# Kernel tuning notes

Measured on AMD Instinct MI355X. Metric: run time of the kernel, lower is better.

## Reference

```python
import jax, jax.numpy as jnp
import numpy as np

N = 200000   # graph nodes
C = 1000     # virtual nodes (clusters)
D = 256      # feature dim (in = hidden = out for this layer)


def setup_inputs() -> dict:
    key = jax.random.key(0)
    ks = jax.random.split(key, 24)
    W = lambda k, shape: jax.random.normal(k, shape, dtype=jnp.float32) * 0.05
    inp = {
        "h": jax.random.normal(ks[0], (N, D), dtype=jnp.float32),
        "g": jax.random.normal(ks[1], (C, D), dtype=jnp.float32),
        "g_hat": jax.random.normal(ks[2], (C, D), dtype=jnp.float32),
        "node2cluster": jax.random.randint(ks[3], (N,), 0, C),
        # AdditiveAttention params (all hidden_dim=D)
        "Wq": W(ks[4], (D, D)),          # query_proj (no bias)
        "Wk": W(ks[5], (D, D)),          # key_proj (no bias)
        "b_attn": jax.random.uniform(ks[6], (D,), jnp.float32, -0.1, 0.1),
        "w_score": W(ks[7], (D,)),       # score_proj weight (D -> 1)
        "b_score": jnp.zeros((), jnp.float32),
        # VNTransmitterUnit.W (D -> D), activation tanh
        "Wv": W(ks[8], (D, D)), "bv": jnp.zeros((D,), jnp.float32),
        # GNTransmitterUnit.F_super (D -> D), tanh
        "Ws": W(ks[9], (D, D)), "bs": jnp.zeros((D,), jnp.float32),
        # gn_merge WarpGateUnit (graph-node side)
        "H1w": W(ks[10], (D, D)), "H1b": jnp.zeros((D,), jnp.float32),
        "G1w": W(ks[11], (D, D)), "G1b": jnp.zeros((D,), jnp.float32),
        # vn_merge WarpGateUnit (virtual-node side)
        "H2w": W(ks[12], (D, D)), "H2b": jnp.zeros((D,), jnp.float32),
        "G2w": W(ks[13], (D, D)), "G2b": jnp.zeros((D,), jnp.float32),
    }
    return inp


def reference(h, g, g_hat, node2cluster,
              Wq, Wk, b_attn, w_score, b_score, Wv, bv, Ws, bs,
              H1w, H1b, G1w, G1b, H2w, H2b, G2w, G2b):
    seg = node2cluster  # (N,) cluster id of each node (the code's vn_index partition)

    # ---- VNTransmitterUnit: segmented additive (Bahdanau) attention, graph -> virtual ----
    # score_proj(tanh(key_proj(cluster_h) + query_proj(g[c]) + bias))
    q = g @ Wq                                             # (C, D)
    k = h @ Wk                                             # (N, D)
    s = jnp.tanh(k + q[seg] + b_attn) @ w_score + b_score  # (N,) per-node score
    # online per-cluster softmax (replaces Python loop over clusters)
    m = jax.ops.segment_max(s, seg, num_segments=C)        # (C,)
    e = jnp.exp(s - m[seg])                                # (N,)
    denom = jax.ops.segment_sum(e, seg, num_segments=C)    # (C,)
    attn = e / denom[seg]                                  # (N,)
    ctx = jax.ops.segment_sum(attn[:, None] * h, seg, num_segments=C)  # (C, D)
    g_trans = jnp.tanh(ctx @ Wv + bv)                      # VNTransmitter: W + tanh

    # ---- GNTransmitterUnit: virtual -> graph, tanh(F_super(g)) then per-node gather ----
    h_trans = jnp.tanh(g @ Ws + bs)                        # (C, D)
    h_trans_n = h_trans[seg]                               # (N, D) index_select by vn_indices[:,1]

    # ---- gn_merge WarpGateUnit: gated fuse on graph nodes ----
    z1 = jax.nn.sigmoid(h @ H1w + H1b + h_trans_n @ G1w + G1b)  # (N, D)
    h_merged = (1.0 - z1) * h + z1 * h_trans_n                   # (N, D)

    # ---- vn_merge WarpGateUnit: gated fuse on virtual nodes (g_hat = vn_update conv out) ----
    z2 = jax.nn.sigmoid(g_trans @ H2w + H2b + g_hat @ G2w + G2b)  # (C, D)
    vx_new = (1.0 - z2) * g_trans + z2 * g_hat                    # (C, D)

    # concat node-side and virtual-side outputs along rows -> (N + C, D)
    return jnp.concatenate([h_merged, vx_new], axis=0)
```

## Files before the change

kernel.cpp:

```cpp
#include <hip/hip_runtime.h>
#include <hip/hip_bf16.h>

#define Nn 200000
#define Cc 1000
#define Dd 256
#define PAD 16
#define NCH7 6250

typedef float f32x16 __attribute__((ext_vector_type(16)));
typedef short bf16x8 __attribute__((ext_vector_type(8)));

#define LOG2E  1.4426950408889634f
#define LOG2E2 2.8853900817779268f

__device__ __forceinline__ unsigned int f2bf(float x){
    union { float f; unsigned int u; } c; c.f = x;
    unsigned int u = c.u;
    u += 0x7fffu + ((u >> 16) & 1u);
    return u >> 16;
}
__device__ __forceinline__ float bf2f(unsigned short b){
    union { unsigned int u; float f; } c; c.u = ((unsigned int)b) << 16;
    return c.f;
}
__device__ __forceinline__ float rcp_(float x){ return __builtin_amdgcn_rcpf(x); }

__global__ void k_prep(const float* __restrict__ Wk, const float* __restrict__ H1w,
                       unsigned short* __restrict__ wfragK, unsigned short* __restrict__ wfragH,
                       int* __restrict__ hist){
    int t = blockIdx.x*256 + threadIdx.x;
    if (t < Cc*PAD) hist[t] = 0;
    int arr = t >> 13;
    int s   = t & 8191;
    int ct  = s >> 10;
    int kk  = (s >> 6) & 15;
    int l   = s & 63;
    int col = ct*32 + (l & 31);
    int k0  = kk*16 + (l >> 5)*8;
    const float* W = arr ? H1w : Wk;
    unsigned short* dst = (arr ? wfragH : wfragK) + (size_t)s*8;
    #pragma unroll
    for (int e = 0; e < 8; ++e) dst[e] = (unsigned short)f2bf(W[(size_t)(k0+e)*Dd + col]);
}

__global__ __launch_bounds__(256)
void k_cluster_prep(const float* __restrict__ g, const float* __restrict__ Wq,
                    const float* __restrict__ b_attn,
                    const float* __restrict__ Ws, const float* __restrict__ bs,
                    const float* __restrict__ G1w, const float* __restrict__ G1b,
                    const float* __restrict__ H1b,
                    const int* __restrict__ seg, int* __restrict__ hist,
                    float* __restrict__ qb, float* __restrict__ h_trans,
                    float* __restrict__ cterm){
    int c0 = blockIdx.x*2, d = threadIdx.x;
    for (int gi = blockIdx.x*256 + d; gi < Nn; gi += 500*256)
        atomicAdd(&hist[seg[gi]*PAD], 1);
    __shared__ float gL[2][Dd], htL[2][Dd];
    gL[0][d] = g[(size_t)c0*Dd + d];
    gL[1][d] = g[(size_t)(c0+1)*Dd + d];
    __syncthreads();
    float ba = b_attn[d], bsv = bs[d];
    float aq0 = ba, aq1 = ba, as0 = bsv, as1 = bsv;
    #pragma unroll 4
    for (int k = 0; k < Dd; ++k){
        float wq = Wq[k*Dd + d], wsv = Ws[k*Dd + d];
        float g0 = gL[0][k], g1 = gL[1][k];
        aq0 = fmaf(g0, wq, aq0);  aq1 = fmaf(g1, wq, aq1);
        as0 = fmaf(g0, wsv, as0); as1 = fmaf(g1, wsv, as1);
    }
    qb[(size_t)c0*Dd + d] = aq0;
    qb[(size_t)(c0+1)*Dd + d] = aq1;
    float ht0 = tanhf(as0), ht1 = tanhf(as1);
    h_trans[(size_t)c0*Dd + d] = ht0;
    h_trans[(size_t)(c0+1)*Dd + d] = ht1;
    htL[0][d] = ht0; htL[1][d] = ht1;
    __syncthreads();
    float bc = H1b[d] + G1b[d];
    float ac0 = bc, ac1 = bc;
    #pragma unroll 4
    for (int k = 0; k < Dd; ++k){
        float gw = G1w[k*Dd + d];
        ac0 = fmaf(htL[0][k], gw, ac0);
        ac1 = fmaf(htL[1][k], gw, ac1);
    }
    cterm[(size_t)c0*Dd + d] = ac0;
    cterm[(size_t)(c0+1)*Dd + d] = ac1;
}

__global__ void k_scan(const int* __restrict__ hist, int* __restrict__ offs, int* __restrict__ cursor){
    __shared__ int sc[1024];
    int t = threadIdx.x;
    int v = (t < Cc) ? hist[t*PAD] : 0;
    sc[t] = v;
    __syncthreads();
    for (int off = 1; off < 1024; off <<= 1){
        int add = (t >= off) ? sc[t - off] : 0;
        __syncthreads();
        sc[t] += add;
        __syncthreads();
    }
    if (t < Cc){
        int excl = sc[t] - v;
        offs[t] = excl;
        cursor[t*PAD] = excl;
    }
}
__global__ void k_scatter(const int* __restrict__ seg, int* __restrict__ cursor, int* __restrict__ order){
    int i = blockIdx.x*256 + threadIdx.x;
    if (i < Nn){
        int p = atomicAdd(&cursor[seg[i]*PAD], 1);
        order[p] = i;
    }
}

__global__ __launch_bounds__(1024, 4)
void k_gemm7(const float* __restrict__ h, const unsigned short* __restrict__ wfrag,
             const int* __restrict__ seg, const float* __restrict__ qb,
             const float* __restrict__ w_score, const float* __restrict__ b_score,
             const float* __restrict__ cterm, const float* __restrict__ h_trans,
             float* __restrict__ e, float* __restrict__ out){
    __shared__ __align__(16) char Al[16384];
    __shared__ float sPart[32][8];
    __shared__ int segL[32];

    int tid = threadIdx.x;
    int w = tid >> 6, l = tid & 63;
    int lCol = l & 31, hiK = l >> 5;
    int rowBase = blockIdx.x * 32;

    {
        const float4* hv = reinterpret_cast<const float4*>(h + (size_t)rowBase * Dd);
        float4 v[2];
        #pragma unroll
        for (int j = 0; j < 2; ++j) v[j] = hv[j*1024 + tid];
        if (tid < 32) segL[tid] = seg[rowBase + tid];
        #pragma unroll
        for (int j = 0; j < 2; ++j){
            int f = j*1024 + tid;
            int row = f >> 6;
            unsigned long long pk = (unsigned long long)f2bf(v[j].x)
                                  | ((unsigned long long)f2bf(v[j].y) << 16)
                                  | ((unsigned long long)f2bf(v[j].z) << 32)
                                  | ((unsigned long long)f2bf(v[j].w) << 48);
            int byte = (row*512 + (f & 63)*8) ^ ((row & 15) << 4);
            *reinterpret_cast<unsigned long long*>(Al + byte) = pk;
        }
    }
    __syncthreads();

    int hOff = lCol*512;
    int swzK = (lCol & 15) << 4;
    const char* wb = reinterpret_cast<const char*>(wfrag) + (size_t)w*16384 + l*16;

    bf16x8 wF[16];
    #pragma unroll
    for (int kk = 0; kk < 16; ++kk)
        wF[kk] = *reinterpret_cast<const bf16x8*>(wb + (size_t)kk*1024);

    f32x16 acc;
    #pragma unroll
    for (int i = 0; i < 16; ++i) acc[i] = 0.f;
    #pragma unroll
    for (int kk = 0; kk < 16; ++kk){
        bf16x8 hF = *reinterpret_cast<const bf16x8*>(Al + ((hOff + kk*32 + hiK*16) ^ swzK));
        acc = __builtin_amdgcn_mfma_f32_32x32x16_bf16(hF, wF[kk], acc, 0, 0, 0);
    }

    if (w < 8){
        float wsc = w_score[w*32 + lCol];
        #pragma unroll
        for (int i = 0; i < 16; ++i){
            int r = (i&3) + 8*(i>>2) + 4*hiK;
            float q = qb[(size_t)segL[r]*Dd + w*32 + lCol];
            float t = exp2f(LOG2E2*(acc[i] + q));
            float p = (t - 1.f)*rcp_(t + 1.f)*wsc;
            p += __shfl_xor(p, 1);
            p += __shfl_xor(p, 2);
            p += __shfl_xor(p, 4);
            p += __shfl_xor(p, 8);
            p += __shfl_xor(p, 16);
            if (lCol == 0) sPart[r][w] = p;
        }
    } else {
        int cb = (w - 8)*32 + lCol;
        #pragma unroll
        for (int i = 0; i < 16; ++i){
            int r = (i&3) + 8*(i>>2) + 4*hiK;
            int sgt = segL[r];
            size_t tb = (size_t)sgt*Dd + cb;
            float c4 = cterm[tb];
            float t4 = h_trans[tb];
            unsigned short hb = *reinterpret_cast<const unsigned short*>(
                Al + ((r*512 + cb*2) ^ ((r & 15) << 4)));
            float hval = bf2f(hb);
            float z = rcp_(1.f + exp2f(-LOG2E*(acc[i] + c4)));
            out[(size_t)(rowBase + r)*Dd + cb] = fmaf(z, t4 - hval, hval);
        }
    }

    __syncthreads();
    if (tid < 32){
        float s = sPart[tid][0] + sPart[tid][1] + sPart[tid][2] + sPart[tid][3]
                + sPart[tid][4] + sPart[tid][5] + sPart[tid][6] + sPart[tid][7] + b_score[0];
        e[rowBase + tid] = exp2f(LOG2E * s);
    }
}

__global__ __launch_bounds__(256)
void k_ctx(const float* __restrict__ h, const float* __restrict__ e,
           const int* __restrict__ order, const int* __restrict__ hist,
           const int* __restrict__ offs,
           float* __restrict__ ctxPart, float* __restrict__ denPart){
    int b = blockIdx.x;
    int c = b >> 2, q = b & 3;
    int cnt = hist[c*PAD], start0 = offs[c];
    int c0 = (cnt * q) >> 2, c1 = (cnt * (q+1)) >> 2;
    int n = c1 - c0;
    int start = start0 + c0;
    int t = threadIdx.x;
    __shared__ int idxL[512];
    __shared__ float eL[512];
    __shared__ float redL[4][256];
    __shared__ float dsum[4];
    int r4 = t >> 6;
    int col4 = (t & 63) << 2;
    float ax = 0.f, ay = 0.f, az = 0.f, aw = 0.f;
    float dpart = 0.f;
    for (int base = 0; base < n; base += 512){
        int m = min(512, n - base);
        for (int i = t; i < m; i += 256){
            int nd = order[start + base + i];
            idxL[i] = nd;
            float ev = e[nd];
            eL[i] = ev;
            dpart += ev;
        }
        __syncthreads();
        #pragma unroll 4
        for (int i = r4; i < m; i += 4){
            float ev = eL[i];
            float4 hv = *reinterpret_cast<const float4*>(h + (size_t)idxL[i]*Dd + col4);
            ax = fmaf(ev, hv.x, ax);
            ay = fmaf(ev, hv.y, ay);
            az = fmaf(ev, hv.z, az);
            aw = fmaf(ev, hv.w, aw);
        }
        __syncthreads();
    }
    *reinterpret_cast<float4*>(&redL[r4][col4]) = (float4){ax, ay, az, aw};
    #pragma unroll
    for (int off = 1; off < 64; off <<= 1) dpart += __shfl_xor(dpart, off);
    if ((t & 63) == 0) dsum[r4] = dpart;
    __syncthreads();
    if (t < 256){
        float s = redL[0][t] + redL[1][t] + redL[2][t] + redL[3][t];
        ctxPart[((size_t)c*4 + q)*Dd + t] = s;
    }
    if (t == 0) denPart[b] = dsum[0] + dsum[1] + dsum[2] + dsum[3];
}

__global__ __launch_bounds__(256)
void k_vn(const float* __restrict__ ctxPart, const float* __restrict__ denPart,
          const float* __restrict__ g_hat,
          const float* __restrict__ Wv, const float* __restrict__ bv,
          const float* __restrict__ H2w, const float* __restrict__ H2b,
          const float* __restrict__ G2w, const float* __restrict__ G2b,
          float* __restrict__ out){
    int c0 = blockIdx.x*2, d = threadIdx.x;
    __shared__ float cL[2][Dd], gtL[2][Dd], ghL[2][Dd];
    #pragma unroll
    for (int j = 0; j < 2; ++j){
        int c = c0 + j;
        float den = denPart[c*4] + denPart[c*4+1] + denPart[c*4+2] + denPart[c*4+3];
        float inv = (den > 0.f) ? 1.f/den : 0.f;
        float num = ctxPart[((size_t)c*4 + 0)*Dd + d] + ctxPart[((size_t)c*4 + 1)*Dd + d]
                  + ctxPart[((size_t)c*4 + 2)*Dd + d] + ctxPart[((size_t)c*4 + 3)*Dd + d];
        cL[j][d]  = num * inv;
        ghL[j][d] = g_hat[(size_t)c*Dd + d];
    }
    __syncthreads();
    float bvv = bv[d];
    float a10 = bvv, a11 = bvv;
    #pragma unroll 4
    for (int k = 0; k < Dd; ++k){
        float wv = Wv[k*Dd + d];
        a10 = fmaf(cL[0][k], wv, a10);
        a11 = fmaf(cL[1][k], wv, a11);
    }
    float gt0 = tanhf(a10), gt1 = tanhf(a11);
    gtL[0][d] = gt0; gtL[1][d] = gt1;
    __syncthreads();
    float b2 = H2b[d] + G2b[d];
    float a20 = b2, a21 = b2;
    #pragma unroll 4
    for (int k = 0; k < Dd; ++k){
        float hw = H2w[k*Dd + d], gw = G2w[k*Dd + d];
        a20 = fmaf(gtL[0][k], hw, a20); a20 = fmaf(ghL[0][k], gw, a20);
        a21 = fmaf(gtL[1][k], hw, a21); a21 = fmaf(ghL[1][k], gw, a21);
    }
    float z0 = 1.f / (1.f + expf(-a20));
    float z1 = 1.f / (1.f + expf(-a21));
    out[(size_t)(Nn + c0)*Dd + d]     = (1.f - z0)*gt0 + z0*ghL[0][d];
    out[(size_t)(Nn + c0 + 1)*Dd + d] = (1.f - z1)*gt1 + z1*ghL[1][d];
}

extern "C" void kernel_launch(void* const* d_in, const int* in_sizes, int n_in,
                              void* d_out, int out_size, void* d_ws, size_t ws_size,
                              hipStream_t stream){
    const float* h       = (const float*)d_in[0];
    const float* g       = (const float*)d_in[1];
    const float* g_hat   = (const float*)d_in[2];
    const int*   seg     = (const int*)  d_in[3];
    const float* Wq      = (const float*)d_in[4];
    const float* Wk      = (const float*)d_in[5];
    const float* b_attn  = (const float*)d_in[6];
    const float* w_score = (const float*)d_in[7];
    const float* b_score = (const float*)d_in[8];
    const float* Wv      = (const float*)d_in[9];
    const float* bv      = (const float*)d_in[10];
    const float* Ws      = (const float*)d_in[11];
    const float* bs      = (const float*)d_in[12];
    const float* H1w     = (const float*)d_in[13];
    const float* H1b     = (const float*)d_in[14];
    const float* G1w     = (const float*)d_in[15];
    const float* G1b     = (const float*)d_in[16];
    const float* H2w     = (const float*)d_in[17];
    const float* H2b     = (const float*)d_in[18];
    const float* G2w     = (const float*)d_in[19];
    const float* G2b     = (const float*)d_in[20];
    float* out = (float*)d_out;

    char* ws = (char*)d_ws;
    unsigned short* wfragK = (unsigned short*)(ws + 0);
    unsigned short* wfragH = (unsigned short*)(ws + 131072);
    float* qb      = (float*)(ws +  262144);
    float* h_trans = (float*)(ws + 1286144);
    float* cterm   = (float*)(ws + 2310144);
    float* e       = (float*)(ws + 3334144);
    int*   order   = (int*)  (ws + 4134144);
    int*   hist    = (int*)  (ws + 4934144);
    int*   offs    = (int*)  (ws + 4998144);
    int*   cursor  = (int*)  (ws + 5002144);
    float* ctxPart = (float*)(ws + 5066144);
    float* denPart = (float*)(ws + 9162144);

    hipLaunchKernelGGL(k_prep, dim3(64), dim3(256), 0, stream, Wk, H1w, wfragK, wfragH, hist);
    hipLaunchKernelGGL(k_cluster_prep, dim3(Cc/2), dim3(256), 0, stream,
                       g, Wq, b_attn, Ws, bs, G1w, G1b, H1b, seg, hist, qb, h_trans, cterm);
    hipLaunchKernelGGL(k_scan, dim3(1), dim3(1024), 0, stream, hist, offs, cursor);
    hipLaunchKernelGGL(k_scatter, dim3((Nn + 255)/256), dim3(256), 0, stream, seg, cursor, order);
    hipLaunchKernelGGL(k_gemm7, dim3(NCH7), dim3(1024), 0, stream,
                       h, wfragK, seg, qb, w_score, b_score, cterm, h_trans, e, out);
    hipLaunchKernelGGL(k_ctx, dim3(Cc*4), dim3(256), 0, stream, h, e, order, hist, offs, ctxPart, denPart);
    hipLaunchKernelGGL(k_vn, dim3(Cc/2), dim3(256), 0, stream,
                       ctxPart, denPart, g_hat, Wv, bv, H2w, H2b, G2w, G2b, out);
}
```

Before: 362.7 us.

## Process 64 rows per GEMM block and pack cterm/h_trans into bf16 pairs

The fused GEMM kernel now handles 64 node rows per block instead of 32. Each wave issues two MFMAs per weight fragment, so every B-fragment load is reused across two row tiles, and the weights are loaded inside the k-loop instead of being held as 16 preloaded registers. The per-cluster cterm and h_trans tables are packed into a single uint32 of two bf16 values, which halves the gather traffic in the gate epilogue at some precision cost. Shared memory per block doubles and the grid halves, which may lower occupancy and latency hiding.

```diff
diff --git a/kernel.cpp b/kernel.cpp
--- a/kernel.cpp
+++ b/kernel.cpp
@@ -5,7 +5,7 @@
 #define Cc 1000
 #define Dd 256
 #define PAD 16
-#define NCH7 6250
+#define NCH8 3125
 
 typedef float f32x16 __attribute__((ext_vector_type(16)));
 typedef short bf16x8 __attribute__((ext_vector_type(8)));
@@ -50,8 +50,7 @@
                     const float* __restrict__ G1w, const float* __restrict__ G1b,
                     const float* __restrict__ H1b,
                     const int* __restrict__ seg, int* __restrict__ hist,
-                    float* __restrict__ qb, float* __restrict__ h_trans,
-                    float* __restrict__ cterm){
+                    float* __restrict__ qb, unsigned int* __restrict__ ctht){
     int c0 = blockIdx.x*2, d = threadIdx.x;
     for (int gi = blockIdx.x*256 + d; gi < Nn; gi += 500*256)
         atomicAdd(&hist[seg[gi]*PAD], 1);
@@ -71,8 +70,6 @@
     qb[(size_t)c0*Dd + d] = aq0;
     qb[(size_t)(c0+1)*Dd + d] = aq1;
     float ht0 = tanhf(as0), ht1 = tanhf(as1);
-    h_trans[(size_t)c0*Dd + d] = ht0;
-    h_trans[(size_t)(c0+1)*Dd + d] = ht1;
     htL[0][d] = ht0; htL[1][d] = ht1;
     __syncthreads();
     float bc = H1b[d] + G1b[d];
@@ -83,8 +80,8 @@
         ac0 = fmaf(htL[0][k], gw, ac0);
         ac1 = fmaf(htL[1][k], gw, ac1);
     }
-    cterm[(size_t)c0*Dd + d] = ac0;
-    cterm[(size_t)(c0+1)*Dd + d] = ac1;
+    ctht[(size_t)c0*Dd + d]     = (f2bf(ac0) << 16) | f2bf(ht0);
+    ctht[(size_t)(c0+1)*Dd + d] = (f2bf(ac1) << 16) | f2bf(ht1);
 }
 
 __global__ void k_scan(const int* __restrict__ hist, int* __restrict__ offs, int* __restrict__ cursor){
@@ -114,28 +111,28 @@
 }
 
 __global__ __launch_bounds__(1024, 4)
-void k_gemm7(const float* __restrict__ h, const unsigned short* __restrict__ wfrag,
+void k_gemm8(const float* __restrict__ h, const unsigned short* __restrict__ wfrag,
              const int* __restrict__ seg, const float* __restrict__ qb,
              const float* __restrict__ w_score, const float* __restrict__ b_score,
-             const float* __restrict__ cterm, const float* __restrict__ h_trans,
+             const unsigned int* __restrict__ ctht,
              float* __restrict__ e, float* __restrict__ out){
-    __shared__ __align__(16) char Al[16384];
-    __shared__ float sPart[32][8];
-    __shared__ int segL[32];
+    __shared__ __align__(16) char Al[32768];
+    __shared__ float sPart[64][8];
+    __shared__ int segL[64];
 
     int tid = threadIdx.x;
     int w = tid >> 6, l = tid & 63;
     int lCol = l & 31, hiK = l >> 5;
-    int rowBase = blockIdx.x * 32;
+    int rowBase = blockIdx.x * 64;
 
     {
         const float4* hv = reinterpret_cast<const float4*>(h + (size_t)rowBase * Dd);
-        float4 v[2];
+        float4 v[4];
         #pragma unroll
-        for (int j = 0; j < 2; ++j) v[j] = hv[j*1024 + tid];
-        if (tid < 32) segL[tid] = seg[rowBase + tid];
+        for (int j = 0; j < 4; ++j) v[j] = hv[j*1024 + tid];
+        if (tid < 64) segL[tid] = seg[rowBase + tid];
         #pragma unroll
-        for (int j = 0; j < 2; ++j){
+        for (int j = 0; j < 4; ++j){
             int f = j*1024 + tid;
             int row = f >> 6;
             unsigned long long pk = (unsigned long long)f2bf(v[j].x)
@@ -152,54 +149,60 @@
     int swzK = (lCol & 15) << 4;
     const char* wb = reinterpret_cast<const char*>(wfrag) + (size_t)w*16384 + l*16;
 
-    bf16x8 wF[16];
-    #pragma unroll
-    for (int kk = 0; kk < 16; ++kk)
-        wF[kk] = *reinterpret_cast<const bf16x8*>(wb + (size_t)kk*1024);
-
-    f32x16 acc;
-    #pragma unroll
-    for (int i = 0; i < 16; ++i) acc[i] = 0.f;
+    f32x16 acc0, acc1;
+    #pragma unroll
+    for (int i = 0; i < 16; ++i){ acc0[i] = 0.f; acc1[i] = 0.f; }
     #pragma unroll
     for (int kk = 0; kk < 16; ++kk){
-        bf16x8 hF = *reinterpret_cast<const bf16x8*>(Al + ((hOff + kk*32 + hiK*16) ^ swzK));
-        acc = __builtin_amdgcn_mfma_f32_32x32x16_bf16(hF, wF[kk], acc, 0, 0, 0);
+        bf16x8 wF = *reinterpret_cast<const bf16x8*>(wb + (size_t)kk*1024);
+        int hb = (hOff + kk*32 + hiK*16) ^ swzK;
+        bf16x8 hF0 = *reinterpret_cast<const bf16x8*>(Al + hb);
+        bf16x8 hF1 = *reinterpret_cast<const bf16x8*>(Al + 16384 + hb);
+        acc0 = __builtin_amdgcn_mfma_f32_32x32x16_bf16(hF0, wF, acc0, 0, 0, 0);
+        acc1 = __builtin_amdgcn_mfma_f32_32x32x16_bf16(hF1, wF, acc1, 0, 0, 0);
     }
 
     if (w < 8){
         float wsc = w_score[w*32 + lCol];
         #pragma unroll
-        for (int i = 0; i < 16; ++i){
-            int r = (i&3) + 8*(i>>2) + 4*hiK;
-            float q = qb[(size_t)segL[r]*Dd + w*32 + lCol];
-            float t = exp2f(LOG2E2*(acc[i] + q));
-            float p = (t - 1.f)*rcp_(t + 1.f)*wsc;
-            p += __shfl_xor(p, 1);
-            p += __shfl_xor(p, 2);
-            p += __shfl_xor(p, 4);
-            p += __shfl_xor(p, 8);
-            p += __shfl_xor(p, 16);
-            if (lCol == 0) sPart[r][w] = p;
+        for (int nt = 0; nt < 2; ++nt){
+            const f32x16& A = nt ? acc1 : acc0;
+            #pragma unroll
+            for (int i = 0; i < 16; ++i){
+                int node = nt*32 + (i&3) + 8*(i>>2) + 4*hiK;
+                float q = qb[(size_t)segL[node]*Dd + w*32 + lCol];
+                float t = exp2f(LOG2E2*(A[i] + q));
+                float p = (t - 1.f)*rcp_(t + 1.f)*wsc;
+                p += __shfl_xor(p, 1);
+                p += __shfl_xor(p, 2);
+                p += __shfl_xor(p, 4);
+                p += __shfl_xor(p, 8);
+                p += __shfl_xor(p, 16);
+                if (lCol == 0) sPart[node][w] = p;
+            }
         }
     } else {
         int cb = (w - 8)*32 + lCol;
         #pragma unroll
-        for (int i = 0; i < 16; ++i){
-            int r = (i&3) + 8*(i>>2) + 4*hiK;
-            int sgt = segL[r];
-            size_t tb = (size_t)sgt*Dd + cb;
-            float c4 = cterm[tb];
-            float t4 = h_trans[tb];
-            unsigned short hb = *reinterpret_cast<const unsigned short*>(
-                Al + ((r*512 + cb*2) ^ ((r & 15) << 4)));
-            float hval = bf2f(hb);
-            float z = rcp_(1.f + exp2f(-LOG2E*(acc[i] + c4)));
-            out[(size_t)(rowBase + r)*Dd + cb] = fmaf(z, t4 - hval, hval);
-        }
-    }
-
-    __syncthreads();
-    if (tid < 32){
+        for (int nt = 0; nt < 2; ++nt){
+            const f32x16& A = nt ? acc1 : acc0;
+            #pragma unroll
+            for (int i = 0; i < 16; ++i){
+                int node = nt*32 + (i&3) + 8*(i>>2) + 4*hiK;
+                unsigned int v = ctht[(size_t)segL[node]*Dd + cb];
+                float c4 = bf2f((unsigned short)(v >> 16));
+                float t4 = bf2f((unsigned short)(v & 0xffff));
+                unsigned short hb = *reinterpret_cast<const unsigned short*>(
+                    Al + ((node*512 + cb*2) ^ ((node & 15) << 4)));
+                float hval = bf2f(hb);
+                float z = rcp_(1.f + exp2f(-LOG2E*(A[i] + c4)));
+                out[(size_t)(rowBase + node)*Dd + cb] = fmaf(z, t4 - hval, hval);
+            }
+        }
+    }
+
+    __syncthreads();
+    if (tid < 64){
         float s = sPart[tid][0] + sPart[tid][1] + sPart[tid][2] + sPart[tid][3]
                 + sPart[tid][4] + sPart[tid][5] + sPart[tid][6] + sPart[tid][7] + b_score[0];
         e[rowBase + tid] = exp2f(LOG2E * s);
@@ -333,24 +336,23 @@
     char* ws = (char*)d_ws;
     unsigned short* wfragK = (unsigned short*)(ws + 0);
     unsigned short* wfragH = (unsigned short*)(ws + 131072);
-    float* qb      = (float*)(ws +  262144);
-    float* h_trans = (float*)(ws + 1286144);
-    float* cterm   = (float*)(ws + 2310144);
-    float* e       = (float*)(ws + 3334144);
-    int*   order   = (int*)  (ws + 4134144);
-    int*   hist    = (int*)  (ws + 4934144);
-    int*   offs    = (int*)  (ws + 4998144);
-    int*   cursor  = (int*)  (ws + 5002144);
-    float* ctxPart = (float*)(ws + 5066144);
-    float* denPart = (float*)(ws + 9162144);
+    float* qb          = (float*)(ws +  262144);
+    unsigned int* ctht = (unsigned int*)(ws + 1286144);
+    float* e       = (float*)(ws + 2310144);
+    int*   order   = (int*)  (ws + 3110144);
+    int*   hist    = (int*)  (ws + 3910144);
+    int*   offs    = (int*)  (ws + 3974144);
+    int*   cursor  = (int*)  (ws + 3978144);
+    float* ctxPart = (float*)(ws + 4042144);
+    float* denPart = (float*)(ws + 8138144);
 
     hipLaunchKernelGGL(k_prep, dim3(64), dim3(256), 0, stream, Wk, H1w, wfragK, wfragH, hist);
     hipLaunchKernelGGL(k_cluster_prep, dim3(Cc/2), dim3(256), 0, stream,
-                       g, Wq, b_attn, Ws, bs, G1w, G1b, H1b, seg, hist, qb, h_trans, cterm);
+                       g, Wq, b_attn, Ws, bs, G1w, G1b, H1b, seg, hist, qb, ctht);
     hipLaunchKernelGGL(k_scan, dim3(1), dim3(1024), 0, stream, hist, offs, cursor);
     hipLaunchKernelGGL(k_scatter, dim3((Nn + 255)/256), dim3(256), 0, stream, seg, cursor, order);
-    hipLaunchKernelGGL(k_gemm7, dim3(NCH7), dim3(1024), 0, stream,
-                       h, wfragK, seg, qb, w_score, b_score, cterm, h_trans, e, out);
+    hipLaunchKernelGGL(k_gemm8, dim3(NCH8), dim3(1024), 0, stream,
+                       h, wfragK, seg, qb, w_score, b_score, ctht, e, out);
     hipLaunchKernelGGL(k_ctx, dim3(Cc*4), dim3(256), 0, stream, h, e, order, hist, offs, ctxPart, denPart);
     hipLaunchKernelGGL(k_vn, dim3(Cc/2), dim3(256), 0, stream,
                        ctxPart, denPart, g_hat, Wv, bv, H2w, H2b, G2w, G2b, out);
```

Result: no change. 358.5 us (-1.2%).
